# Performance work log

Measured on AMD Instinct MI355X. Metric: run time of the kernel, lower is better.

Reference implementation:

```python
import jax, jax.numpy as jnp
import numpy as np

TEMP = 0.1
COEFF = 0.5
WARMUP = 0
S = 32 * 32  # hardcoded in the torch module


def _l2n(x, axis):
    # matches F.normalize(p=2, eps=1e-12)
    n = jnp.linalg.norm(x, axis=axis, keepdims=True)
    return x / jnp.maximum(n, 1e-12)


def _ce_first_class(pos, neg):
    # cross-entropy with label 0 on logits = [pos | neg] / T
    logits = jnp.concatenate([pos, neg], axis=1) / TEMP
    return jnp.mean(jax.nn.logsumexp(logits, axis=1) - logits[:, 0])


def _dense_losses(q_of, q_x, k_of, k_x, k_avg_dense):
    # q_of,k_of: (B,d,S) normalized; q_x,k_x: (B,C,S) normalized; k_avg_dense: (B,C) UN-normalized (torch bug preserved)
    B, C, _ = q_x.shape
    sim = jnp.einsum('bds,bdt->bst', q_of, k_of)          # (B,S,S)
    ind = jnp.argmax(sim, axis=2)                          # (B,S)
    idxg = jnp.take_along_axis(k_x, jnp.broadcast_to(ind[:, None, :], k_x.shape), axis=2)
    idxg = jax.lax.stop_gradient(idxg)                     # computed under torch.no_grad
    l_pos = jnp.sum(q_x * idxg, axis=1).reshape(-1, 1)     # (B*S,1)
    qf = jnp.transpose(q_x, (0, 2, 1)).reshape(-1, C)      # (B*S,C)
    l_neg_full = qf @ k_avg_dense.T                        # (B*S,B)
    # static mask: row n excludes column n // S
    base = np.stack([np.delete(np.arange(B), i) for i in range(B)])  # (B,B-1)
    neg_cols = jnp.asarray(np.repeat(base, S, axis=0))     # (B*S,B-1)
    l_neg = jnp.take_along_axis(l_neg_full, neg_cols, axis=1)
    return l_pos, l_neg


def _forward(original_features_q, avgpooled_global_q, x_q, avgpooled_dense_q,
             original_features_k, avgpooled_global_k, x_k, avgpooled_dense_k, epoch):
    of = jnp.concatenate([original_features_q, original_features_k], axis=0)
    ag = jnp.concatenate([avgpooled_global_q, avgpooled_global_k], axis=0)
    x = jnp.concatenate([x_q, x_k], axis=0)
    ad = jnp.concatenate([avgpooled_dense_q, avgpooled_dense_k], axis=0)

    # global InfoNCE
    agn = _l2n(ag, 1)
    sim = agn @ agn.T                                      # (2B,2B)
    n2 = sim.shape[0]
    B = n2 // 2
    rows = np.arange(n2)
    pos_cols = (rows + B) % n2
    pos = sim[jnp.asarray(rows), jnp.asarray(pos_cols)][:, None]
    neg_cols = np.stack([np.setdiff1d(rows, [i, pos_cols[i]]) for i in range(n2)])  # (2B,2B-2)
    neg = jnp.take_along_axis(sim, jnp.asarray(neg_cols), axis=1)
    global_loss = _ce_first_class(pos, neg)

    # dense InfoNCE
    b, d, h, w = of.shape
    of = _l2n(of.reshape(b, d, h * w), 1)
    xn = _l2n(x, 1)
    q_of, k_of = of[:b // 2], of[b // 2:]
    q_x, k_x = xn[:b // 2], xn[b // 2:]
    q_ad, k_ad = ad[:b // 2], ad[b // 2:]  # NOTE: un-normalized, matching the torch code
    p1, n1 = _dense_losses(q_of, q_x, k_of, k_x, k_ad)
    p2, n2_ = _dense_losses(k_of, k_x, q_of, q_x, q_ad)
    dense_loss = _ce_first_class(jnp.concatenate([p1, p2], axis=0),
                                 jnp.concatenate([n1, n2_], axis=0))

    if epoch > WARMUP:
        return COEFF * global_loss + (1.0 - COEFF) * dense_loss
    return global_loss


def setup_inputs() -> dict:
    key = jax.random.key(0)
    ks = jax.random.split(key, 8)
    B, d, C, h, w = 64, 256, 128, 32, 32
    return {
        'original_features_q': jax.random.normal(ks[0], (B, d, h, w), jnp.float32),
        'avgpooled_global_q': jax.random.normal(ks[1], (B, C), jnp.float32),
        'x_q': jax.random.normal(ks[2], (B, C, h * w), jnp.float32),
        'avgpooled_dense_q': jax.random.normal(ks[3], (B, C), jnp.float32),
        'original_features_k': jax.random.normal(ks[4], (B, d, h, w), jnp.float32),
        'avgpooled_global_k': jax.random.normal(ks[5], (B, C), jnp.float32),
        'x_k': jax.random.normal(ks[6], (B, C, h * w), jnp.float32),
        'avgpooled_dense_k': jax.random.normal(ks[7], (B, C), jnp.float32),
        'epoch': 5,
    }


def reference(original_features_q, avgpooled_global_q, x_q, avgpooled_dense_q,
              original_features_k, avgpooled_global_k, x_k, avgpooled_dense_k, epoch):
    return _forward(original_features_q, avgpooled_global_q, x_q, avgpooled_dense_q,
                    original_features_k, avgpooled_global_k, x_k, avgpooled_dense_k, epoch)
```

## Files before the change

### kernel.cpp

```cpp
#include <hip/hip_runtime.h>
#include <math.h>

#define TEMP_INV 10.0f

typedef unsigned long long u64;
typedef __attribute__((ext_vector_type(8))) __bf16 bf16x8;
typedef __attribute__((ext_vector_type(4))) float f32x4;

__device__ inline unsigned fkey(float v) {
  unsigned u = __float_as_uint(v);
  return (u & 0x80000000u) ? ~u : (u | 0x80000000u);
}

__device__ __forceinline__ void async_copy16(const void* gp, void* lp) {
  __builtin_amdgcn_global_load_lds(
      (__attribute__((address_space(1))) void*)(unsigned long long)gp,
      (__attribute__((address_space(3))) void*)(unsigned long long)lp,
      16, 0, 0);
}

__global__ __launch_bounds__(256) void kpre(
    const float* __restrict__ ofq, const float* __restrict__ ofk,
    __bf16* __restrict__ ofT, float* __restrict__ of_invn,
    const float* __restrict__ xq, const float* __restrict__ xk,
    float* __restrict__ x_invn,
    const float* __restrict__ adq, const float* __restrict__ adk,
    float* __restrict__ adt,
    const float* __restrict__ agq, const float* __restrict__ agk,
    float* __restrict__ gsum) {
  unsigned bx = blockIdx.x;
  int t = threadIdx.x;
  if (bx < 4096) {
    int s0 = (bx & 31) * 32, b = bx >> 5;
    const float* src = (b < 64) ? (ofq + (size_t)b * 262144) : (ofk + (size_t)(b - 64) * 262144);
    __shared__ __bf16 T[8][32][36];
    __shared__ float R[8][32];
    int dd = t >> 5, ss = t & 31;
    int wr = t >> 3, wd = t & 7;
    float v[8][4];
#pragma unroll
    for (int d0i = 0; d0i < 8; ++d0i)
#pragma unroll
      for (int it = 0; it < 4; ++it)
        v[d0i][it] = src[(size_t)(d0i * 32 + dd + 8 * it) * 1024 + s0 + ss];
    float ssq = 0.f;
#pragma unroll
    for (int d0i = 0; d0i < 8; ++d0i)
#pragma unroll
      for (int it = 0; it < 4; ++it) ssq += v[d0i][it] * v[d0i][it];
#pragma unroll
    for (int d0i = 0; d0i < 8; ++d0i)
#pragma unroll
      for (int it = 0; it < 4; ++it) T[d0i][ss][dd + 8 * it] = (__bf16)v[d0i][it];
    R[dd][ss] = ssq;
    __syncthreads();
    __bf16* out = ofT + (size_t)b * 262144 + (size_t)s0 * 256;
#pragma unroll
    for (int d0i = 0; d0i < 8; ++d0i)
      *(uint2*)(out + (size_t)wr * 256 + d0i * 32 + wd * 4) = *(const uint2*)(&T[d0i][wr][wd * 4]);
    if (t < 32) {
      float a = 0.f;
#pragma unroll
      for (int r = 0; r < 8; ++r) a += R[r][t];
      of_invn[b * 1024 + s0 + t] = 1.0f / fmaxf(sqrtf(a), 1e-12f);
    }
  } else if (bx < 4672) {
    unsigned px = bx - 4096;
    if (px < 512) {
      int idx = px * 256 + t;
      int b = idx >> 10, s = idx & 1023;
      const float* src = (b < 64) ? (xq + (size_t)b * 131072) : (xk + (size_t)(b - 64) * 131072);
      float acc = 0.f;
#pragma unroll 8
      for (int c = 0; c < 128; ++c) { float v = src[c * 1024 + s]; acc += v * v; }
      x_invn[idx] = 1.0f / fmaxf(sqrtf(acc), 1e-12f);
    } else {
      int i = (px - 512) * 256 + t;
      int dir = i >> 13, r = i & 8191;
      int j = r >> 7, c = r & 127;
      const float* ad = dir == 0 ? adk : adq;
      adt[dir * 8192 + c * 64 + j] = ad[j * 128 + c];
    }
  } else {
    __shared__ float logits[2][128];
    __shared__ float rinv[128];
    int ii = t >> 7, j = t & 127;
    int i = (int)(bx - 4672) * 2 + ii;
    const float* rowi = (i < 64) ? (agq + i * 128) : (agk + (i - 64) * 128);
    const float* rowj = (j < 64) ? (agq + j * 128) : (agk + (j - 64) * 128);
    float dot = 0.f, nj = 0.f;
#pragma unroll 8
    for (int c = 0; c < 128; ++c) { float a = rowi[c], bb = rowj[c]; dot += a * bb; nj += bb * bb; }
    if (ii == 0) rinv[j] = 1.0f / fmaxf(sqrtf(nj), 1e-12f);
    __syncthreads();
    logits[ii][j] = dot * rinv[i] * rinv[j] * TEMP_INV;
    __syncthreads();
    if (j == 0) {
      int pos = (i + 64) & 127;
      float m = -INFINITY;
      for (int tt = 0; tt < 128; ++tt) if (tt != i) m = fmaxf(m, logits[ii][tt]);
      float e = 0.f;
      for (int tt = 0; tt < 128; ++tt) if (tt != i) e += __expf(logits[ii][tt] - m);
      atomicAdd(gsum, m + __logf(e) - logits[ii][pos]);
    }
  }
}

__global__ __launch_bounds__(512, 2) void ksim(
    const __bf16* __restrict__ ofT, const float* __restrict__ of_invn,
    u64* __restrict__ best_row, u64* __restrict__ best_col) {
  unsigned h = blockIdx.x + (blockIdx.y << 2) + (blockIdx.z << 4);
  int xcd = h & 7;
  unsigned slot = h >> 3;
  int b = xcd + 8 * (int)(slot >> 4);
  int tile = slot & 15;
  int s0 = (tile & 3) * 256, t0 = (tile >> 2) * 256;

  const __bf16* Ag = ofT + (size_t)b * 262144;
  const __bf16* Bg = ofT + (size_t)(b + 64) * 262144;
  __shared__ __bf16 As[2][16384];
  __shared__ __bf16 Bs[2][16384];

  int t = threadIdx.x;
  int lane = t & 63, w = t >> 6;
  int lc = lane & 15, q = lane >> 4;
  int wm = w >> 2, wn = w & 3;

  f32x4 acc[8][4];
#pragma unroll
  for (int i = 0; i < 8; ++i)
#pragma unroll
    for (int j = 0; j < 4; ++j) acc[i][j] = (f32x4)(0.f);

  int aoff[8], boff[4];
#pragma unroll
  for (int i = 0; i < 8; ++i) {
    int mr = wm * 128 + i * 16 + lc;
    aoff[i] = mr * 64 + ((q ^ (mr & 7)) << 3);
  }
#pragma unroll
  for (int j = 0; j < 4; ++j) {
    int nc = wn * 64 + j * 16 + lc;
    boff[j] = nc * 64 + ((q ^ (nc & 7)) << 3);
  }

  int ms = t >> 3, gphys = t & 7;
  int lg = gphys ^ (ms & 7);
  size_t aSrc = (size_t)(s0 + ms) * 256 + lg * 8;
  size_t bSrc = (size_t)(t0 + ms) * 256 + lg * 8;

  auto STAGE = [&](int bufn, int k0) {
    char* aL = (char*)&As[bufn][0] + t * 16;
    char* bL = (char*)&Bs[bufn][0] + t * 16;
#pragma unroll
    for (int c = 0; c < 4; ++c) {
      async_copy16(Ag + aSrc + (size_t)c * 16384 + k0, aL + c * 8192);
      async_copy16(Bg + bSrc + (size_t)c * 16384 + k0, bL + c * 8192);
    }
  };

  STAGE(0, 0);
  __syncthreads();

  for (int it = 0; it < 4; ++it) {
    int buf = it & 1;
    if (it < 3) STAGE(buf ^ 1, (it + 1) * 64);
#pragma unroll
    for (int kk = 0; kk < 2; ++kk) {
      int kx = kk << 5;
      bf16x8 af[8], bfr[4];
#pragma unroll
      for (int i = 0; i < 8; ++i) af[i] = *(const bf16x8*)(&As[buf][0] + (aoff[i] ^ kx));
#pragma unroll
      for (int j = 0; j < 4; ++j) bfr[j] = *(const bf16x8*)(&Bs[buf][0] + (boff[j] ^ kx));
      __builtin_amdgcn_s_setprio(1);
#pragma unroll
      for (int i = 0; i < 8; ++i)
#pragma unroll
        for (int j = 0; j < 4; ++j)
          acc[i][j] = __builtin_amdgcn_mfma_f32_16x16x32_bf16(af[i], bfr[j], acc[i][j], 0, 0, 0);
      __builtin_amdgcn_s_setprio(0);
    }
    __syncthreads();
  }

  float sk[4];
#pragma unroll
  for (int j = 0; j < 4; ++j) sk[j] = of_invn[65536 + b * 1024 + t0 + wn * 64 + j * 16 + lc];
  float sq[32];
#pragma unroll
  for (int i = 0; i < 8; ++i)
#pragma unroll
    for (int e = 0; e < 4; ++e)
      sq[i * 4 + e] = of_invn[b * 1024 + s0 + wm * 128 + i * 16 + q * 4 + e];

  u64* browb = best_row + (size_t)b * 1024 + s0;
  u64* bcolb = best_col + (size_t)b * 1024 + t0;

#pragma unroll
  for (int i = 0; i < 8; ++i) {
#pragma unroll
    for (int e = 0; e < 4; ++e) {
      float v[4];
#pragma unroll
      for (int j = 0; j < 4; ++j) v[j] = acc[i][j][e] * sk[j];
      float vb = fmaxf(fmaxf(v[0], v[1]), fmaxf(v[2], v[3]));
#pragma unroll
      for (int mask = 1; mask <= 8; mask <<= 1) vb = fmaxf(vb, __shfl_xor(vb, mask));
      unsigned ib = 0xFFFFFFFFu;
#pragma unroll
      for (int j = 0; j < 4; ++j) {
        unsigned cand = (v[j] == vb) ? (unsigned)(t0 + wn * 64 + j * 16 + lc) : 0xFFFFFFFFu;
        ib = min(ib, cand);
      }
#pragma unroll
      for (int mask = 1; mask <= 8; mask <<= 1) ib = min(ib, __shfl_xor(ib, mask));
      if (lc == 0)
        atomicMax(browb + wm * 128 + i * 16 + q * 4 + e,
                  ((u64)fkey(vb) << 32) | (u64)(0xFFFFFFFFu - ib));
    }
  }

#pragma unroll
  for (int j = 0; j < 4; ++j) {
    float cb = -INFINITY;
#pragma unroll
    for (int i = 0; i < 8; ++i)
#pragma unroll
      for (int e = 0; e < 4; ++e) cb = fmaxf(cb, acc[i][j][e] * sq[i * 4 + e]);
    cb = fmaxf(cb, __shfl_xor(cb, 16));
    cb = fmaxf(cb, __shfl_xor(cb, 32));
    unsigned ib = 0xFFFFFFFFu;
#pragma unroll
    for (int i = 0; i < 8; ++i)
#pragma unroll
      for (int e = 0; e < 4; ++e) {
        float m2 = acc[i][j][e] * sq[i * 4 + e];
        unsigned cand = (m2 == cb) ? (unsigned)(s0 + wm * 128 + i * 16 + q * 4 + e) : 0xFFFFFFFFu;
        ib = min(ib, cand);
      }
    ib = min(ib, __shfl_xor(ib, 16));
    ib = min(ib, __shfl_xor(ib, 32));
    if (lane < 16)
      atomicMax(bcolb + wn * 64 + j * 16 + lane,
                ((u64)fkey(cb) << 32) | (u64)(0xFFFFFFFFu - ib));
  }
}

__global__ __launch_bounds__(1024) void kpos(
    const float* __restrict__ xq, const float* __restrict__ xk,
    const float* __restrict__ x_invn,
    const u64* __restrict__ best_row, const u64* __restrict__ best_col,
    float* __restrict__ posl) {
  int b = blockIdx.x, dir = blockIdx.y;
  const float* xsrc = dir == 0 ? xq : xk;
  const float* xdst = dir == 0 ? xk : xq;
  const float* inv_src = x_invn + (dir ? 65536 : 0);
  const float* inv_dst = x_invn + (dir ? 0 : 65536);
  const u64* best = dir == 0 ? best_row : best_col;

  __shared__ float xrow[8][1024];
  __shared__ float sdinv[1024];
  int t = threadIdx.x;
  sdinv[t] = inv_dst[b * 1024 + t];
  u64 p = best[(size_t)b * 1024 + t];
  int sidx = (int)(0xFFFFFFFFu - (unsigned)(p & 0xFFFFFFFFull));
  const float* xsb = xsrc + (size_t)b * 131072;
  const float* xdb = xdst + (size_t)b * 131072;
  float acc = 0.f;
  for (int c0 = 0; c0 < 128; c0 += 8) {
    __syncthreads();
#pragma unroll
    for (int qq = 0; qq < 2; ++qq)
      ((float4*)xrow)[t + 1024 * qq] = ((const float4*)(xdb + (size_t)c0 * 1024))[t + 1024 * qq];
    __syncthreads();
#pragma unroll
    for (int cc = 0; cc < 8; ++cc)
      acc += xsb[(size_t)(c0 + cc) * 1024 + t] * xrow[cc][sidx];
  }
  posl[dir * 65536 + b * 1024 + t] = acc * inv_src[b * 1024 + t] * sdinv[sidx] * TEMP_INV;
}

__global__ __launch_bounds__(256) void kneg(
    const float* __restrict__ xq, const float* __restrict__ xk,
    const float* __restrict__ x_invn,
    const float* __restrict__ adt, const float* __restrict__ posl,
    float* __restrict__ dsum) {
  int st = blockIdx.x, b = blockIdx.y, dir = blockIdx.z;
  const float* xsrc = dir == 0 ? xq : xk;
  const float* inv_src = x_invn + (dir ? 65536 : 0);
  const float* Bt = adt + dir * 8192;

  __shared__ float As2[64][64];
  __shared__ float Bs2[128][64];
  __shared__ float red[16];

  int tid = threadIdx.x;
  int tx = tid & 15, ty = tid >> 4;
  int s0 = st * 64;

#pragma unroll
  for (int qq = 0; qq < 8; ++qq)
    reinterpret_cast<float4*>(Bs2)[tid + 256 * qq] =
        reinterpret_cast<const float4*>(Bt)[tid + 256 * qq];

  float acc[4][4];
#pragma unroll
  for (int i = 0; i < 4; ++i)
#pragma unroll
    for (int j = 0; j < 4; ++j) acc[i][j] = 0.f;

  int lm = tid & 63, lk = tid >> 6;
  float sinv = inv_src[b * 1024 + s0 + lm];
  const float* xb = xsrc + (size_t)b * 131072;

  for (int k0 = 0; k0 < 128; k0 += 64) {
#pragma unroll
    for (int r = 0; r < 16; ++r) {
      int kk = lk + 4 * r;
      As2[kk][lm] = xb[(k0 + kk) * 1024 + s0 + lm] * sinv;
    }
    __syncthreads();
#pragma unroll
    for (int kk = 0; kk < 64; ++kk) {
      float4 av = *reinterpret_cast<const float4*>(&As2[kk][ty * 4]);
      float4 bv = *reinterpret_cast<const float4*>(&Bs2[k0 + kk][tx * 4]);
      float a[4] = {av.x, av.y, av.z, av.w};
      float bb[4] = {bv.x, bv.y, bv.z, bv.w};
#pragma unroll
      for (int i = 0; i < 4; ++i)
#pragma unroll
        for (int j = 0; j < 4; ++j) acc[i][j] += a[i] * bb[j];
    }
    __syncthreads();
  }

  float lsum = 0.f;
#pragma unroll
  for (int i = 0; i < 4; ++i) {
    int s = s0 + ty * 4 + i;
    float pos = posl[dir * 65536 + b * 1024 + s];
    float lg[4];
    float mloc = -INFINITY;
#pragma unroll
    for (int j = 0; j < 4; ++j) {
      int jg = tx * 4 + j;
      lg[j] = (jg == b) ? -INFINITY : acc[i][j] * TEMP_INV;
      mloc = fmaxf(mloc, lg[j]);
    }
#pragma unroll
    for (int mask = 1; mask <= 8; mask <<= 1) mloc = fmaxf(mloc, __shfl_xor(mloc, mask));
    float m = fmaxf(mloc, pos);
    float e = 0.f;
#pragma unroll
    for (int j = 0; j < 4; ++j) e += __expf(lg[j] - m);
#pragma unroll
    for (int mask = 1; mask <= 8; mask <<= 1) e += __shfl_xor(e, mask);
    if (tx == 0) lsum += m + __logf(e + __expf(pos - m)) - pos;
  }
  if (tx == 0) red[ty] = lsum;
  __syncthreads();
  if (tid == 0) {
    float v = 0.f;
#pragma unroll
    for (int r = 0; r < 16; ++r) v += red[r];
    atomicAdd(dsum, v);
  }
}

__global__ void kfinal(const float* __restrict__ gsum, const float* __restrict__ dsum,
                       const int* __restrict__ epoch, float* __restrict__ out) {
  if (threadIdx.x == 0) {
    float g = gsum[0] / 128.0f;
    float dn = dsum[0] / 131072.0f;
    out[0] = (epoch[0] > 0) ? (0.5f * g + 0.5f * dn) : g;
  }
}

extern "C" void kernel_launch(void* const* d_in, const int* in_sizes, int n_in,
                              void* d_out, int out_size, void* d_ws, size_t ws_size,
                              hipStream_t stream) {
  const float* ofq = (const float*)d_in[0];
  const float* agq = (const float*)d_in[1];
  const float* xq  = (const float*)d_in[2];
  const float* adq = (const float*)d_in[3];
  const float* ofk = (const float*)d_in[4];
  const float* agk = (const float*)d_in[5];
  const float* xk  = (const float*)d_in[6];
  const float* adk = (const float*)d_in[7];
  const int* epoch = (const int*)d_in[8];
  float* out = (float*)d_out;

  char* wsb = (char*)d_ws;
  __bf16* ofT = (__bf16*)wsb;
  u64* best_row = (u64*)(wsb + 67108864);
  u64* best_col = best_row + 65536;
  float* gsum = (float*)(best_col + 65536);
  float* dsum = gsum + 1;
  float* posl = dsum + 1;
  float* x_invn  = posl + 131072;
  float* of_invn = x_invn + 131072;
  float* adt = of_invn + 131072;

  hipMemsetAsync(best_row, 0, 65536ull * 8 * 2 + 8, stream);

  kpre<<<4736, 256, 0, stream>>>(ofq, ofk, ofT, of_invn, xq, xk, x_invn,
                                 adq, adk, adt, agq, agk, gsum);

  dim3 gs(4, 4, 64);
  ksim<<<gs, 512, 0, stream>>>(ofT, of_invn, best_row, best_col);

  dim3 gp(64, 2);
  kpos<<<gp, 1024, 0, stream>>>(xq, xk, x_invn, best_row, best_col, posl);

  dim3 gn(16, 64, 2);
  kneg<<<gn, 256, 0, stream>>>(xq, xk, x_invn, adt, posl, dsum);

  kfinal<<<1, 1, 0, stream>>>(gsum, dsum, epoch, out);
}
```

Baseline: 385.5 us.

## Split preprocessing, reorder batches for L2 reuse, halve kpos blocks, fuse final

The fused preprocessing kernel is split in two. The bf16 transpose/convert kernel now orders batches by XCD and pairs q with k, while ksim walks batches in reverse, so the most recently converted data is more likely still in cache. The x-norm, adt and global-loss work moves after ksim, kpos is split into two 512-thread halves per batch for more blocks, and kfinal is folded into kneg through a last-block atomic counter. The aim is better L2 locality between kernels and one fewer launch, at the cost of extra atomics and fences.

```diff
diff --git a/kernel.cpp b/kernel.cpp
--- a/kernel.cpp
+++ b/kernel.cpp
@@ -19,9 +19,52 @@
       16, 0, 0);
 }
 
-__global__ __launch_bounds__(256) void kpre(
-    const float* __restrict__ ofq, const float* __restrict__ ofk,
-    __bf16* __restrict__ ofT, float* __restrict__ of_invn,
+__global__ __launch_bounds__(256) void kcvt(const float* __restrict__ ofq,
+                                            const float* __restrict__ ofk,
+                                            __bf16* __restrict__ ofT,
+                                            float* __restrict__ of_invn) {
+  unsigned bx = blockIdx.x;
+  int t = threadIdx.x;
+  int xcd = bx & 7;
+  unsigned idx = bx >> 3;
+  int j = idx >> 5;
+  int s0 = (idx & 31) * 32;
+  int b = xcd + 8 * (j >> 1) + 64 * (j & 1);
+  const float* src = (b < 64) ? (ofq + (size_t)b * 262144) : (ofk + (size_t)(b - 64) * 262144);
+  __shared__ __bf16 T[8][32][36];
+  __shared__ float R[8][32];
+  int dd = t >> 5, ss = t & 31;
+  int wr = t >> 3, wd = t & 7;
+  float v[8][4];
+#pragma unroll
+  for (int d0i = 0; d0i < 8; ++d0i)
+#pragma unroll
+    for (int it = 0; it < 4; ++it)
+      v[d0i][it] = src[(size_t)(d0i * 32 + dd + 8 * it) * 1024 + s0 + ss];
+  float ssq = 0.f;
+#pragma unroll
+  for (int d0i = 0; d0i < 8; ++d0i)
+#pragma unroll
+    for (int it = 0; it < 4; ++it) ssq += v[d0i][it] * v[d0i][it];
+#pragma unroll
+  for (int d0i = 0; d0i < 8; ++d0i)
+#pragma unroll
+    for (int it = 0; it < 4; ++it) T[d0i][ss][dd + 8 * it] = (__bf16)v[d0i][it];
+  R[dd][ss] = ssq;
+  __syncthreads();
+  __bf16* out = ofT + (size_t)b * 262144 + (size_t)s0 * 256;
+#pragma unroll
+  for (int d0i = 0; d0i < 8; ++d0i)
+    *(uint2*)(out + (size_t)wr * 256 + d0i * 32 + wd * 4) = *(const uint2*)(&T[d0i][wr][wd * 4]);
+  if (t < 32) {
+    float a = 0.f;
+#pragma unroll
+    for (int r = 0; r < 8; ++r) a += R[r][t];
+    of_invn[b * 1024 + s0 + t] = 1.0f / fmaxf(sqrtf(a), 1e-12f);
+  }
+}
+
+__global__ __launch_bounds__(256) void kpre2(
     const float* __restrict__ xq, const float* __restrict__ xk,
     float* __restrict__ x_invn,
     const float* __restrict__ adq, const float* __restrict__ adk,
@@ -30,72 +73,35 @@
     float* __restrict__ gsum) {
   unsigned bx = blockIdx.x;
   int t = threadIdx.x;
-  if (bx < 4096) {
-    int s0 = (bx & 31) * 32, b = bx >> 5;
-    const float* src = (b < 64) ? (ofq + (size_t)b * 262144) : (ofk + (size_t)(b - 64) * 262144);
-    __shared__ __bf16 T[8][32][36];
-    __shared__ float R[8][32];
-    int dd = t >> 5, ss = t & 31;
-    int wr = t >> 3, wd = t & 7;
-    float v[8][4];
-#pragma unroll
-    for (int d0i = 0; d0i < 8; ++d0i)
-#pragma unroll
-      for (int it = 0; it < 4; ++it)
-        v[d0i][it] = src[(size_t)(d0i * 32 + dd + 8 * it) * 1024 + s0 + ss];
-    float ssq = 0.f;
-#pragma unroll
-    for (int d0i = 0; d0i < 8; ++d0i)
-#pragma unroll
-      for (int it = 0; it < 4; ++it) ssq += v[d0i][it] * v[d0i][it];
-#pragma unroll
-    for (int d0i = 0; d0i < 8; ++d0i)
-#pragma unroll
-      for (int it = 0; it < 4; ++it) T[d0i][ss][dd + 8 * it] = (__bf16)v[d0i][it];
-    R[dd][ss] = ssq;
-    __syncthreads();
-    __bf16* out = ofT + (size_t)b * 262144 + (size_t)s0 * 256;
-#pragma unroll
-    for (int d0i = 0; d0i < 8; ++d0i)
-      *(uint2*)(out + (size_t)wr * 256 + d0i * 32 + wd * 4) = *(const uint2*)(&T[d0i][wr][wd * 4]);
-    if (t < 32) {
-      float a = 0.f;
-#pragma unroll
-      for (int r = 0; r < 8; ++r) a += R[r][t];
-      of_invn[b * 1024 + s0 + t] = 1.0f / fmaxf(sqrtf(a), 1e-12f);
-    }
-  } else if (bx < 4672) {
-    unsigned px = bx - 4096;
-    if (px < 512) {
-      int idx = px * 256 + t;
-      int b = idx >> 10, s = idx & 1023;
-      const float* src = (b < 64) ? (xq + (size_t)b * 131072) : (xk + (size_t)(b - 64) * 131072);
-      float acc = 0.f;
+  if (bx < 512) {
+    int idx = bx * 256 + t;
+    int b = idx >> 10, s = idx & 1023;
+    const float* src = (b < 64) ? (xq + (size_t)b * 131072) : (xk + (size_t)(b - 64) * 131072);
+    float acc = 0.f;
 #pragma unroll 8
-      for (int c = 0; c < 128; ++c) { float v = src[c * 1024 + s]; acc += v * v; }
-      x_invn[idx] = 1.0f / fmaxf(sqrtf(acc), 1e-12f);
-    } else {
-      int i = (px - 512) * 256 + t;
-      int dir = i >> 13, r = i & 8191;
-      int j = r >> 7, c = r & 127;
-      const float* ad = dir == 0 ? adk : adq;
-      adt[dir * 8192 + c * 64 + j] = ad[j * 128 + c];
-    }
+    for (int c = 0; c < 128; ++c) { float v = src[c * 1024 + s]; acc += v * v; }
+    x_invn[idx] = 1.0f / fmaxf(sqrtf(acc), 1e-12f);
+  } else if (bx < 576) {
+    int i = (bx - 512) * 256 + t;
+    int dir = i >> 13, r = i & 8191;
+    int jj = r >> 7, c = r & 127;
+    const float* ad = dir == 0 ? adk : adq;
+    adt[dir * 8192 + c * 64 + jj] = ad[jj * 128 + c];
   } else {
     __shared__ float logits[2][128];
     __shared__ float rinv[128];
-    int ii = t >> 7, j = t & 127;
-    int i = (int)(bx - 4672) * 2 + ii;
+    int ii = t >> 7, jl = t & 127;
+    int i = (int)(bx - 576) * 2 + ii;
     const float* rowi = (i < 64) ? (agq + i * 128) : (agk + (i - 64) * 128);
-    const float* rowj = (j < 64) ? (agq + j * 128) : (agk + (j - 64) * 128);
+    const float* rowj = (jl < 64) ? (agq + jl * 128) : (agk + (jl - 64) * 128);
     float dot = 0.f, nj = 0.f;
 #pragma unroll 8
     for (int c = 0; c < 128; ++c) { float a = rowi[c], bb = rowj[c]; dot += a * bb; nj += bb * bb; }
-    if (ii == 0) rinv[j] = 1.0f / fmaxf(sqrtf(nj), 1e-12f);
-    __syncthreads();
-    logits[ii][j] = dot * rinv[i] * rinv[j] * TEMP_INV;
-    __syncthreads();
-    if (j == 0) {
+    if (ii == 0) rinv[jl] = 1.0f / fmaxf(sqrtf(nj), 1e-12f);
+    __syncthreads();
+    logits[ii][jl] = dot * rinv[i] * rinv[jl] * TEMP_INV;
+    __syncthreads();
+    if (jl == 0) {
       int pos = (i + 64) & 127;
       float m = -INFINITY;
       for (int tt = 0; tt < 128; ++tt) if (tt != i) m = fmaxf(m, logits[ii][tt]);
@@ -112,7 +118,7 @@
   unsigned h = blockIdx.x + (blockIdx.y << 2) + (blockIdx.z << 4);
   int xcd = h & 7;
   unsigned slot = h >> 3;
-  int b = xcd + 8 * (int)(slot >> 4);
+  int b = xcd + 8 * (7 - (int)(slot >> 4));
   int tile = slot & 15;
   int s0 = (tile & 3) * 256, t0 = (tile >> 2) * 256;
 
@@ -247,12 +253,12 @@
   }
 }
 
-__global__ __launch_bounds__(1024) void kpos(
+__global__ __launch_bounds__(512) void kpos(
     const float* __restrict__ xq, const float* __restrict__ xk,
     const float* __restrict__ x_invn,
     const u64* __restrict__ best_row, const u64* __restrict__ best_col,
     float* __restrict__ posl) {
-  int b = blockIdx.x, dir = blockIdx.y;
+  int b = blockIdx.x, dir = blockIdx.y, half = blockIdx.z;
   const float* xsrc = dir == 0 ? xq : xk;
   const float* xdst = dir == 0 ? xk : xq;
   const float* inv_src = x_invn + (dir ? 65536 : 0);
@@ -262,8 +268,10 @@
   __shared__ float xrow[8][1024];
   __shared__ float sdinv[1024];
   int t = threadIdx.x;
+  int s = half * 512 + t;
   sdinv[t] = inv_dst[b * 1024 + t];
-  u64 p = best[(size_t)b * 1024 + t];
+  sdinv[t + 512] = inv_dst[b * 1024 + t + 512];
+  u64 p = best[(size_t)b * 1024 + s];
   int sidx = (int)(0xFFFFFFFFu - (unsigned)(p & 0xFFFFFFFFull));
   const float* xsb = xsrc + (size_t)b * 131072;
   const float* xdb = xdst + (size_t)b * 131072;
@@ -271,21 +279,22 @@
   for (int c0 = 0; c0 < 128; c0 += 8) {
     __syncthreads();
 #pragma unroll
-    for (int qq = 0; qq < 2; ++qq)
-      ((float4*)xrow)[t + 1024 * qq] = ((const float4*)(xdb + (size_t)c0 * 1024))[t + 1024 * qq];
+    for (int qq = 0; qq < 4; ++qq)
+      ((float4*)xrow)[t + 512 * qq] = ((const float4*)(xdb + (size_t)c0 * 1024))[t + 512 * qq];
     __syncthreads();
 #pragma unroll
     for (int cc = 0; cc < 8; ++cc)
-      acc += xsb[(size_t)(c0 + cc) * 1024 + t] * xrow[cc][sidx];
-  }
-  posl[dir * 65536 + b * 1024 + t] = acc * inv_src[b * 1024 + t] * sdinv[sidx] * TEMP_INV;
+      acc += xsb[(size_t)(c0 + cc) * 1024 + s] * xrow[cc][sidx];
+  }
+  posl[dir * 65536 + b * 1024 + s] = acc * inv_src[b * 1024 + s] * sdinv[sidx] * TEMP_INV;
 }
 
 __global__ __launch_bounds__(256) void kneg(
     const float* __restrict__ xq, const float* __restrict__ xk,
     const float* __restrict__ x_invn,
     const float* __restrict__ adt, const float* __restrict__ posl,
-    float* __restrict__ dsum) {
+    float* __restrict__ gsum, float* __restrict__ dsum, unsigned* __restrict__ cnt,
+    const int* __restrict__ epoch, float* __restrict__ out) {
   int st = blockIdx.x, b = blockIdx.y, dir = blockIdx.z;
   const float* xsrc = dir == 0 ? xq : xk;
   const float* inv_src = x_invn + (dir ? 65536 : 0);
@@ -365,15 +374,14 @@
 #pragma unroll
     for (int r = 0; r < 16; ++r) v += red[r];
     atomicAdd(dsum, v);
-  }
-}
-
-__global__ void kfinal(const float* __restrict__ gsum, const float* __restrict__ dsum,
-                       const int* __restrict__ epoch, float* __restrict__ out) {
-  if (threadIdx.x == 0) {
-    float g = gsum[0] / 128.0f;
-    float dn = dsum[0] / 131072.0f;
-    out[0] = (epoch[0] > 0) ? (0.5f * g + 0.5f * dn) : g;
+    __threadfence();
+    unsigned old = atomicAdd(cnt, 1u);
+    if (old == 2047u) {
+      __threadfence();
+      float g = atomicAdd(gsum, 0.0f) / 128.0f;
+      float dn = atomicAdd(dsum, 0.0f) / 131072.0f;
+      out[0] = (epoch[0] > 0) ? (0.5f * g + 0.5f * dn) : g;
+    }
   }
 }
 
@@ -397,24 +405,24 @@
   u64* best_col = best_row + 65536;
   float* gsum = (float*)(best_col + 65536);
   float* dsum = gsum + 1;
-  float* posl = dsum + 1;
+  unsigned* cnt = (unsigned*)(dsum + 1);
+  float* posl = (float*)(cnt + 2);
   float* x_invn  = posl + 131072;
   float* of_invn = x_invn + 131072;
   float* adt = of_invn + 131072;
 
-  hipMemsetAsync(best_row, 0, 65536ull * 8 * 2 + 8, stream);
-
-  kpre<<<4736, 256, 0, stream>>>(ofq, ofk, ofT, of_invn, xq, xk, x_invn,
-                                 adq, adk, adt, agq, agk, gsum);
+  hipMemsetAsync(best_row, 0, 65536ull * 8 * 2 + 16, stream);
+
+  kcvt<<<4096, 256, 0, stream>>>(ofq, ofk, ofT, of_invn);
 
   dim3 gs(4, 4, 64);
   ksim<<<gs, 512, 0, stream>>>(ofT, of_invn, best_row, best_col);
 
-  dim3 gp(64, 2);
-  kpos<<<gp, 1024, 0, stream>>>(xq, xk, x_invn, best_row, best_col, posl);
+  kpre2<<<640, 256, 0, stream>>>(xq, xk, x_invn, adq, adk, adt, agq, agk, gsum);
+
+  dim3 gp(64, 2, 2);
+  kpos<<<gp, 512, 0, stream>>>(xq, xk, x_invn, best_row, best_col, posl);
 
   dim3 gn(16, 64, 2);
-  kneg<<<gn, 256, 0, stream>>>(xq, xk, x_invn, adt, posl, dsum);
-
-  kfinal<<<1, 1, 0, stream>>>(gsum, dsum, epoch, out);
-}
+  kneg<<<gn, 256, 0, stream>>>(xq, xk, x_invn, adt, posl, gsum, dsum, cnt, epoch, out);
+}
```

After: 412.0 us. 1.07x slower.

## Fold x norm computation into kpos and remap conversion blocks across XCDs

Applied to the files above, without the earlier changes.

Removes the separate x-norm pass from the preprocessing kernel. kpos now accumulates the squared norms of the source and gathered destination channels during its dot-product loop and writes the source inverse norm for kneg. This saves a full extra read of x_q and x_k. The conversion kernel's block-to-batch mapping is also changed so blocks on the same XCD write the batches that ksim later reads there, and ksim walks batches in reverse order, presumably to reuse data still in L2. The gathered-destination norm is now taken from the gathered values rather than a precomputed table, which is mathematically equivalent.

```diff
diff --git a/kernel.cpp b/kernel.cpp
--- a/kernel.cpp
+++ b/kernel.cpp
@@ -19,19 +19,24 @@
       16, 0, 0);
 }
 
-__global__ __launch_bounds__(256) void kpre(
-    const float* __restrict__ ofq, const float* __restrict__ ofk,
-    __bf16* __restrict__ ofT, float* __restrict__ of_invn,
-    const float* __restrict__ xq, const float* __restrict__ xk,
-    float* __restrict__ x_invn,
-    const float* __restrict__ adq, const float* __restrict__ adk,
-    float* __restrict__ adt,
-    const float* __restrict__ agq, const float* __restrict__ agk,
-    float* __restrict__ gsum) {
+__global__ __launch_bounds__(256) void kcvt(const float* __restrict__ ofq,
+                                            const float* __restrict__ ofk,
+                                            __bf16* __restrict__ ofT,
+                                            float* __restrict__ of_invn,
+                                            const float* __restrict__ adq,
+                                            const float* __restrict__ adk,
+                                            float* __restrict__ adt,
+                                            const float* __restrict__ agq,
+                                            const float* __restrict__ agk,
+                                            float* __restrict__ gsum) {
   unsigned bx = blockIdx.x;
   int t = threadIdx.x;
   if (bx < 4096) {
-    int s0 = (bx & 31) * 32, b = bx >> 5;
+    int xcd = bx & 7;
+    unsigned idx = bx >> 3;
+    int j = idx >> 5;
+    int s0 = (idx & 31) * 32;
+    int b = xcd + 8 * (j >> 1) + 64 * (j & 1);
     const float* src = (b < 64) ? (ofq + (size_t)b * 262144) : (ofk + (size_t)(b - 64) * 262144);
     __shared__ __bf16 T[8][32][36];
     __shared__ float R[8][32];
@@ -64,38 +69,27 @@
       for (int r = 0; r < 8; ++r) a += R[r][t];
       of_invn[b * 1024 + s0 + t] = 1.0f / fmaxf(sqrtf(a), 1e-12f);
     }
-  } else if (bx < 4672) {
-    unsigned px = bx - 4096;
-    if (px < 512) {
-      int idx = px * 256 + t;
-      int b = idx >> 10, s = idx & 1023;
-      const float* src = (b < 64) ? (xq + (size_t)b * 131072) : (xk + (size_t)(b - 64) * 131072);
-      float acc = 0.f;
-#pragma unroll 8
-      for (int c = 0; c < 128; ++c) { float v = src[c * 1024 + s]; acc += v * v; }
-      x_invn[idx] = 1.0f / fmaxf(sqrtf(acc), 1e-12f);
-    } else {
-      int i = (px - 512) * 256 + t;
-      int dir = i >> 13, r = i & 8191;
-      int j = r >> 7, c = r & 127;
-      const float* ad = dir == 0 ? adk : adq;
-      adt[dir * 8192 + c * 64 + j] = ad[j * 128 + c];
-    }
+  } else if (bx < 4160) {
+    int i = (int)(bx - 4096) * 256 + t;
+    int dir = i >> 13, r = i & 8191;
+    int jj = r >> 7, c = r & 127;
+    const float* ad = dir == 0 ? adk : adq;
+    adt[dir * 8192 + c * 64 + jj] = ad[jj * 128 + c];
   } else {
     __shared__ float logits[2][128];
     __shared__ float rinv[128];
-    int ii = t >> 7, j = t & 127;
-    int i = (int)(bx - 4672) * 2 + ii;
+    int ii = t >> 7, jl = t & 127;
+    int i = (int)(bx - 4160) * 2 + ii;
     const float* rowi = (i < 64) ? (agq + i * 128) : (agk + (i - 64) * 128);
-    const float* rowj = (j < 64) ? (agq + j * 128) : (agk + (j - 64) * 128);
+    const float* rowj = (jl < 64) ? (agq + jl * 128) : (agk + (jl - 64) * 128);
     float dot = 0.f, nj = 0.f;
 #pragma unroll 8
     for (int c = 0; c < 128; ++c) { float a = rowi[c], bb = rowj[c]; dot += a * bb; nj += bb * bb; }
-    if (ii == 0) rinv[j] = 1.0f / fmaxf(sqrtf(nj), 1e-12f);
-    __syncthreads();
-    logits[ii][j] = dot * rinv[i] * rinv[j] * TEMP_INV;
-    __syncthreads();
-    if (j == 0) {
+    if (ii == 0) rinv[jl] = 1.0f / fmaxf(sqrtf(nj), 1e-12f);
+    __syncthreads();
+    logits[ii][jl] = dot * rinv[i] * rinv[jl] * TEMP_INV;
+    __syncthreads();
+    if (jl == 0) {
       int pos = (i + 64) & 127;
       float m = -INFINITY;
       for (int tt = 0; tt < 128; ++tt) if (tt != i) m = fmaxf(m, logits[ii][tt]);
@@ -112,7 +106,7 @@
   unsigned h = blockIdx.x + (blockIdx.y << 2) + (blockIdx.z << 4);
   int xcd = h & 7;
   unsigned slot = h >> 3;
-  int b = xcd + 8 * (int)(slot >> 4);
+  int b = xcd + 8 * (7 - (int)(slot >> 4));
   int tile = slot & 15;
   int s0 = (tile & 3) * 256, t0 = (tile >> 2) * 256;
 
@@ -249,25 +243,21 @@
 
 __global__ __launch_bounds__(1024) void kpos(
     const float* __restrict__ xq, const float* __restrict__ xk,
-    const float* __restrict__ x_invn,
+    float* __restrict__ x_invn,
     const u64* __restrict__ best_row, const u64* __restrict__ best_col,
     float* __restrict__ posl) {
   int b = blockIdx.x, dir = blockIdx.y;
   const float* xsrc = dir == 0 ? xq : xk;
   const float* xdst = dir == 0 ? xk : xq;
-  const float* inv_src = x_invn + (dir ? 65536 : 0);
-  const float* inv_dst = x_invn + (dir ? 0 : 65536);
   const u64* best = dir == 0 ? best_row : best_col;
 
   __shared__ float xrow[8][1024];
-  __shared__ float sdinv[1024];
   int t = threadIdx.x;
-  sdinv[t] = inv_dst[b * 1024 + t];
   u64 p = best[(size_t)b * 1024 + t];
   int sidx = (int)(0xFFFFFFFFu - (unsigned)(p & 0xFFFFFFFFull));
   const float* xsb = xsrc + (size_t)b * 131072;
   const float* xdb = xdst + (size_t)b * 131072;
-  float acc = 0.f;
+  float acc = 0.f, ssq_s = 0.f, ssq_d = 0.f;
   for (int c0 = 0; c0 < 128; c0 += 8) {
     __syncthreads();
 #pragma unroll
@@ -275,10 +265,18 @@
       ((float4*)xrow)[t + 1024 * qq] = ((const float4*)(xdb + (size_t)c0 * 1024))[t + 1024 * qq];
     __syncthreads();
 #pragma unroll
-    for (int cc = 0; cc < 8; ++cc)
-      acc += xsb[(size_t)(c0 + cc) * 1024 + t] * xrow[cc][sidx];
-  }
-  posl[dir * 65536 + b * 1024 + t] = acc * inv_src[b * 1024 + t] * sdinv[sidx] * TEMP_INV;
+    for (int cc = 0; cc < 8; ++cc) {
+      float a_ = xsb[(size_t)(c0 + cc) * 1024 + t];
+      float d_ = xrow[cc][sidx];
+      acc += a_ * d_;
+      ssq_s += a_ * a_;
+      ssq_d += d_ * d_;
+    }
+  }
+  float invs = 1.0f / fmaxf(sqrtf(ssq_s), 1e-12f);
+  float invd = 1.0f / fmaxf(sqrtf(ssq_d), 1e-12f);
+  posl[dir * 65536 + b * 1024 + t] = acc * invs * invd * TEMP_INV;
+  x_invn[(dir ? 65536 : 0) + b * 1024 + t] = invs;
 }
 
 __global__ __launch_bounds__(256) void kneg(
@@ -404,8 +402,7 @@
 
   hipMemsetAsync(best_row, 0, 65536ull * 8 * 2 + 8, stream);
 
-  kpre<<<4736, 256, 0, stream>>>(ofq, ofk, ofT, of_invn, xq, xk, x_invn,
-                                 adq, adk, adt, agq, agk, gsum);
+  kcvt<<<4224, 256, 0, stream>>>(ofq, ofk, ofT, of_invn, adq, adk, adt, agq, agk, gsum);
 
   dim3 gs(4, 4, 64);
   ksim<<<gs, 512, 0, stream>>>(ofT, of_invn, best_row, best_col);
```

Result: no change. 385.9 us (+0.1%).
